# Performance work log

Hardware: AMD Instinct MI355X
Metric: run time of the kernel (lower is better)

## Reference

```python
import jax, jax.numpy as jnp
import numpy as np

NUM_CLASSES = 80
INF = 1e8
STRIDES = (8, 16, 32, 64, 128)
REG = ((0.0, 64.0), (64.0, 128.0), (128.0, 256.0), (256.0, 512.0), (512.0, INF))
GRAY_F = (0.9, 1.1)
FM = ((128, 128), (64, 64), (32, 32), (16, 16), (8, 8))  # 1024x1024 input


def _build_level_constants():
    pts, rr, gr, st = [], [], [], []
    for (h, w), s, (lo, up) in zip(FM, STRIDES, REG):
        xs = np.arange(w, dtype=np.float32) * s
        ys = np.arange(h, dtype=np.float32) * s
        ym, xm = np.meshgrid(ys, xs, indexing='ij')
        n = h * w
        pts.append(np.stack([xm.ravel(), ym.ravel()], axis=-1))
        rr.append(np.tile(np.array([lo, up], np.float32), (n, 1)))
        gr.append(np.tile(np.array([lo * GRAY_F[0], up * GRAY_F[1]], np.float32), (n, 1)))
        st.append(np.full((n,), s, np.float32))
    cat = lambda a: jnp.asarray(np.concatenate(a, axis=0))
    return cat(pts), cat(rr), cat(gr), cat(st)


def setup_inputs() -> dict:
    key = jax.random.key(0)
    k1, k2, k3, k4 = jax.random.split(key, 4)
    B, G = 8, 100
    x0 = jax.random.uniform(k1, (B, G, 1), minval=0.0, maxval=900.0)
    y0 = jax.random.uniform(k2, (B, G, 1), minval=0.0, maxval=900.0)
    wh = jax.random.uniform(k3, (B, G, 2), minval=8.0, maxval=512.0)
    gt_bboxes = jnp.concatenate([x0, y0, wh], axis=-1)  # xywh
    gt_labels = jax.random.randint(k4, (B, G), 0, NUM_CLASSES)
    points, reg_ranges, gray_ranges, strides = _build_level_constants()
    return dict(gt_bboxes=gt_bboxes, gt_labels=gt_labels, points=points,
                reg_ranges=reg_ranges, gray_ranges=gray_ranges, strides=strides)


def _single_image(gt_bboxes, gt_labels, points, reg_ranges, gray_ranges, strides):
    # gt_bboxes [G,4] (x,y,w,h); points [P,2]; returns [P, C+4]
    px = points[:, 0:1]                      # [P,1]
    py = points[:, 1:2]
    x0 = gt_bboxes[None, :, 0]               # [1,G]
    y0 = gt_bboxes[None, :, 1]
    w = gt_bboxes[None, :, 2]
    h = gt_bboxes[None, :, 3]
    cx = x0 + w / 2.0
    cy = y0 + h / 2.0
    half = strides[:, None] / 2.0            # [P,1]

    xs = jnp.abs(px - cx) / half
    xs = jnp.where(xs >= 1.0, xs, 1.0)       # == xs*(xs>=1) + (xs<1)
    ys = jnp.abs(py - cy) / half
    ys = jnp.where(ys >= 1.0, ys, 1.0)
    scores = jnp.sqrt(1.0 / xs) * jnp.sqrt(1.0 / ys)   # [P,G]

    dx1 = px - x0
    dy1 = py - y0
    dx2 = x0 + w - 1.0 - px
    dy2 = y0 + h - 1.0 - py
    delta = jnp.stack([dx1, dy1, dx2, dy2], axis=-1)   # [P,G,4]
    delta = delta / reg_ranges[:, 1][:, None, None]

    larger = jnp.maximum(w, h)               # [1,G]
    lo, up = reg_ranges[:, 0:1], reg_ranges[:, 1:2]      # [P,1]
    glo, gup = gray_ranges[:, 0:1], gray_ranges[:, 1:2]
    hit = jnp.min(delta, axis=-1) >= 0       # [P,G]
    green = (lo <= larger) & (larger <= up) & hit
    gray = (((glo <= larger) & (larger < lo)) | ((up < larger) & (larger <= gup))) & hit

    order = jnp.argsort(scores, axis=1)      # ascending, like torch.sort
    s_scores = jnp.take_along_axis(scores, order, axis=1)
    s_labels = jnp.take_along_axis(jnp.broadcast_to(gt_labels[None, :], scores.shape), order, axis=1)
    s_green = jnp.take_along_axis(green, order, axis=1)
    s_gray = jnp.take_along_axis(gray, order, axis=1)
    s_delta = jnp.take_along_axis(delta, order[..., None], axis=1)

    P = points.shape[0]
    rows = jnp.broadcast_to(jnp.arange(P)[:, None], s_labels.shape)
    cls = jnp.zeros((P, NUM_CLASSES), scores.dtype)
    cls = cls.at[rows, s_labels].max(jnp.where(s_green, s_scores, 0.0))
    gray_hit = jnp.zeros((P, NUM_CLASSES), scores.dtype)
    gray_hit = gray_hit.at[rows, s_labels].max(s_gray.astype(scores.dtype))
    cls = jnp.where(gray_hit > 0, -1.0, cls)  # gray writes happen after green

    filt = s_scores * (s_green & ~s_gray)
    sel = jnp.argmax(filt, axis=1)            # first max, like torch.max
    reg = jnp.take_along_axis(s_delta, sel[:, None, None], axis=1)[:, 0, :]  # [P,4]
    return jnp.concatenate([cls, reg], axis=-1)


def reference(gt_bboxes, gt_labels, points, reg_ranges, gray_ranges, strides):
    f = jax.vmap(lambda b, l: _single_image(b, l, points, reg_ranges, gray_ranges, strides))
    return f(gt_bboxes, gt_labels)
```

## Files before the change

### kernel.cpp

```cpp
#include <hip/hip_runtime.h>

#define ROWF 84

__global__ __launch_bounds__(256) void lfd_zero_kernel(float4* __restrict__ dst, int n4) {
    const int stride = gridDim.x * blockDim.x;
    const float4 z = make_float4(0.f, 0.f, 0.f, 0.f);
    for (int i = blockIdx.x * blockDim.x + threadIdx.x; i < n4; i += stride)
        dst[i] = z;
}

__global__ __launch_bounds__(64) void lfd_patch_kernel(
    const float* __restrict__ gt_bboxes,
    const int*   __restrict__ gt_labels,
    const float* __restrict__ points,
    const float* __restrict__ reg_ranges,
    const float* __restrict__ gray_ranges,
    const float* __restrict__ strides,
    float* __restrict__ out,
    int G, int P)
{
    extern __shared__ float lds[];
    float4*   boxA  = (float4*)lds;
    float2*   ctr   = (float2*)(boxA + G);
    unsigned* clist = (unsigned*)(ctr + ((G + 1) & ~1));

    const int tid = threadIdx.x;
    const int b   = blockIdx.y;
    const int p   = blockIdx.x * 64 + tid;

    const float px  = points[p * 2 + 0];
    const float py  = points[p * 2 + 1];
    const float lo  = reg_ranges[p * 2 + 0];
    const float up  = reg_ranges[p * 2 + 1];
    const float glo = gray_ranges[p * 2 + 0];
    const float gup = gray_ranges[p * 2 + 1];
    const float inv_half = 2.0f / strides[p];
    const float inv_up   = 1.0f / up;

    bool i0 = false, gray0 = false, i1 = false, gray1 = false;
    int  lab0 = 0, lab1 = 0;
    {
        int g = tid;
        if (g < G) {
            const float4 bb = *(const float4*)(gt_bboxes + (size_t)(b * G + g) * 4);
            boxA[g] = make_float4(bb.x, bb.y, bb.x + bb.z - 1.0f, bb.y + bb.w - 1.0f);
            ctr[g]  = make_float2(bb.x + 0.5f * bb.z, bb.y + 0.5f * bb.w);
            const float larger = fmaxf(bb.z, bb.w);
            lab0 = gt_labels[b * G + g];
            const bool green = (lo <= larger) && (larger <= up);
            gray0 = ((glo <= larger) && (larger < lo)) || ((up < larger) && (larger <= gup));
            i0 = green || gray0;
        }
        g = tid + 64;
        if (g < G) {
            const float4 bb = *(const float4*)(gt_bboxes + (size_t)(b * G + g) * 4);
            boxA[g] = make_float4(bb.x, bb.y, bb.x + bb.z - 1.0f, bb.y + bb.w - 1.0f);
            ctr[g]  = make_float2(bb.x + 0.5f * bb.z, bb.y + 0.5f * bb.w);
            const float larger = fmaxf(bb.z, bb.w);
            lab1 = gt_labels[b * G + g];
            const bool green = (lo <= larger) && (larger <= up);
            gray1 = ((glo <= larger) && (larger < lo)) || ((up < larger) && (larger <= gup));
            i1 = green || gray1;
        }
    }
    const unsigned long long m0 = __ballot(i0);
    const unsigned long long m1 = __ballot(i1);
    const int c0 = __popcll(m0);
    const unsigned long long below = (1ull << tid) - 1ull;
    if (i0) clist[__popcll(m0 & below)] =
        (unsigned)tid | ((unsigned)lab0 << 8) | (gray0 ? 0x80000000u : 0u);
    if (i1) clist[c0 + __popcll(m1 & below)] =
        (unsigned)(tid + 64) | ((unsigned)lab1 << 8) | (gray1 ? 0x80000000u : 0u);
    const int ncomp = c0 + __popcll(m1);

#define SC(X, Y) rsqrtf(fmaxf(fabsf(px - (X)) * inv_half, 1.0f) * \
                        fmaxf(fabsf(py - (Y)) * inv_half, 1.0f))
    const float4* ctr2 = (const float4*)ctr;
    float ms0 = 1e30f, ms1 = 1e30f, ms2 = 1e30f, ms3 = 1e30f;
    int   mg0 = 0, mg1 = 0, mg2 = 0, mg3 = 0;
    int g = 0;
    for (; g + 8 <= G; g += 8) {
        const float4 ca = ctr2[(g >> 1) + 0];
        const float4 cb = ctr2[(g >> 1) + 1];
        const float4 cc = ctr2[(g >> 1) + 2];
        const float4 cd = ctr2[(g >> 1) + 3];
        float s;
        s = SC(ca.x, ca.y); if (s < ms0) { ms0 = s; mg0 = g + 0; }
        s = SC(ca.z, ca.w); if (s < ms0) { ms0 = s; mg0 = g + 1; }
        s = SC(cb.x, cb.y); if (s < ms1) { ms1 = s; mg1 = g + 2; }
        s = SC(cb.z, cb.w); if (s < ms1) { ms1 = s; mg1 = g + 3; }
        s = SC(cc.x, cc.y); if (s < ms2) { ms2 = s; mg2 = g + 4; }
        s = SC(cc.z, cc.w); if (s < ms2) { ms2 = s; mg2 = g + 5; }
        s = SC(cd.x, cd.y); if (s < ms3) { ms3 = s; mg3 = g + 6; }
        s = SC(cd.z, cd.w); if (s < ms3) { ms3 = s; mg3 = g + 7; }
    }
    for (; g + 2 <= G; g += 2) {
        const float4 ca = ctr2[g >> 1];
        float s;
        s = SC(ca.x, ca.y); if (s < ms0) { ms0 = s; mg0 = g; }
        s = SC(ca.z, ca.w); if (s < ms0) { ms0 = s; mg0 = g + 1; }
    }
    if (g < G) {
        const float2 c = ctr[g];
        const float s = SC(c.x, c.y);
        if (s < ms0) { ms0 = s; mg0 = g; }
    }
    float min_score = ms0; int min_g = mg0;
    if (ms1 < min_score || (ms1 == min_score && mg1 < min_g)) { min_score = ms1; min_g = mg1; }
    if (ms2 < min_score || (ms2 == min_score && mg2 < min_g)) { min_score = ms2; min_g = mg2; }
    if (ms3 < min_score || (ms3 == min_score && mg3 < min_g)) { min_score = ms3; min_g = mg3; }

    float* myout = out + ((size_t)b * P + p) * ROWF;
    float best_score = 0.f; int best_g = 0;
    unsigned gm0 = 0u, gm1 = 0u, gm2 = 0u;
    for (int i = 0; i < ncomp; ++i) {
        const unsigned e = clist[i];
        const int gg = (int)(e & 0xFFu);
        const float4 A = boxA[gg];
        const float d1 = px - A.x, d2 = py - A.y, d3 = A.z - px, d4 = A.w - py;
        if (fminf(fminf(d1, d2), fminf(d3, d4)) >= 0.0f) {
            const int label = (int)((e >> 8) & 0x7Fu);
            if (e & 0x80000000u) {
                if (label < 32)      gm0 |= 1u << label;
                else if (label < 64) gm1 |= 1u << (label - 32);
                else                 gm2 |= 1u << (label - 64);
            } else {
                const float2 c = ctr[gg];
                const float s = SC(c.x, c.y);
                atomicMax((int*)(myout + label), __float_as_int(s));
                if (s > best_score) { best_score = s; best_g = gg; }
            }
        }
    }
#undef SC

    asm volatile("s_waitcnt vmcnt(0)" ::: "memory");

    unsigned t;
    t = gm0; while (t) { const int c = __ffs(t) - 1; myout[c]      = -1.0f; t &= t - 1u; }
    t = gm1; while (t) { const int c = __ffs(t) - 1; myout[32 + c] = -1.0f; t &= t - 1u; }
    t = gm2; while (t) { const int c = __ffs(t) - 1; myout[64 + c] = -1.0f; t &= t - 1u; }

    const int sel = (best_score > 0.f) ? best_g : min_g;
    const float4 A = boxA[sel];
    *(float4*)(myout + 80) = make_float4((px - A.x) * inv_up, (py - A.y) * inv_up,
                                         (A.z - px) * inv_up, (A.w - py) * inv_up);
}

extern "C" void kernel_launch(void* const* d_in, const int* in_sizes, int n_in,
                              void* d_out, int out_size, void* d_ws, size_t ws_size,
                              hipStream_t stream) {
    const float* gt_bboxes   = (const float*)d_in[0];
    const int*   gt_labels   = (const int*)d_in[1];
    const float* points      = (const float*)d_in[2];
    const float* reg_ranges  = (const float*)d_in[3];
    const float* gray_ranges = (const float*)d_in[4];
    const float* strides     = (const float*)d_in[5];
    float* out = (float*)d_out;

    const int P = in_sizes[5];
    const int B = out_size / (P * ROWF);
    const int G = in_sizes[1] / B;

    const int n4 = out_size / 4;
    lfd_zero_kernel<<<1024, 256, 0, stream>>>((float4*)out, n4);

    dim3 grid(P / 64, B);
    dim3 block(64);
    const size_t shmem = (size_t)G * sizeof(float4)
                       + (size_t)((G + 1) & ~1) * sizeof(float2)
                       + (size_t)G * sizeof(unsigned);
    lfd_patch_kernel<<<grid, block, shmem, stream>>>(
        gt_bboxes, gt_labels, points, reg_ranges, gray_ranges, strides, out, G, P);
}
```

Baseline: 41.98 us.

## Fuse zero-fill into main kernel with LDS-staged coalesced row writes

Removes the separate zero-fill kernel and the per-label global atomicMax/scatter writes. Each thread records hit and gray bitmasks plus regression targets in LDS. The block then writes its full output tile with coalesced float4 stores, recomputing per-class max scores from the bitmasks. This avoids writing the output twice and avoids scattered atomics, in exchange for redundant score recomputation and extra LDS use.

```diff
diff --git a/kernel.cpp b/kernel.cpp
--- a/kernel.cpp
+++ b/kernel.cpp
@@ -1,15 +1,9 @@
 #include <hip/hip_runtime.h>
 
 #define ROWF 84
-
-__global__ __launch_bounds__(256) void lfd_zero_kernel(float4* __restrict__ dst, int n4) {
-    const int stride = gridDim.x * blockDim.x;
-    const float4 z = make_float4(0.f, 0.f, 0.f, 0.f);
-    for (int i = blockIdx.x * blockDim.x + threadIdx.x; i < n4; i += stride)
-        dst[i] = z;
-}
-
-__global__ __launch_bounds__(64) void lfd_patch_kernel(
+#define RSTRIDE 17
+
+__global__ __launch_bounds__(64) void lfd_kernel(
     const float* __restrict__ gt_bboxes,
     const int*   __restrict__ gt_labels,
     const float* __restrict__ points,
@@ -23,6 +17,7 @@
     float4*   boxA  = (float4*)lds;
     float2*   ctr   = (float2*)(boxA + G);
     unsigned* clist = (unsigned*)(ctr + ((G + 1) & ~1));
+    unsigned* rowd  = clist + G;
 
     const int tid = threadIdx.x;
     const int b   = blockIdx.y;
@@ -110,9 +105,9 @@
     if (ms2 < min_score || (ms2 == min_score && mg2 < min_g)) { min_score = ms2; min_g = mg2; }
     if (ms3 < min_score || (ms3 == min_score && mg3 < min_g)) { min_score = ms3; min_g = mg3; }
 
-    float* myout = out + ((size_t)b * P + p) * ROWF;
+    unsigned hm0 = 0u, hm1 = 0u, hm2 = 0u, hm3 = 0u;
+    unsigned gm0 = 0u, gm1 = 0u, gm2 = 0u;
     float best_score = 0.f; int best_g = 0;
-    unsigned gm0 = 0u, gm1 = 0u, gm2 = 0u;
     for (int i = 0; i < ncomp; ++i) {
         const unsigned e = clist[i];
         const int gg = (int)(e & 0xFFu);
@@ -125,26 +120,77 @@
                 else if (label < 64) gm1 |= 1u << (label - 32);
                 else                 gm2 |= 1u << (label - 64);
             } else {
+                if (i < 32)       hm0 |= 1u << i;
+                else if (i < 64)  hm1 |= 1u << (i - 32);
+                else if (i < 96)  hm2 |= 1u << (i - 64);
+                else              hm3 |= 1u << (i - 96);
                 const float2 c = ctr[gg];
                 const float s = SC(c.x, c.y);
-                atomicMax((int*)(myout + label), __float_as_int(s));
                 if (s > best_score) { best_score = s; best_g = gg; }
             }
         }
     }
-#undef SC
-
-    asm volatile("s_waitcnt vmcnt(0)" ::: "memory");
-
-    unsigned t;
-    t = gm0; while (t) { const int c = __ffs(t) - 1; myout[c]      = -1.0f; t &= t - 1u; }
-    t = gm1; while (t) { const int c = __ffs(t) - 1; myout[32 + c] = -1.0f; t &= t - 1u; }
-    t = gm2; while (t) { const int c = __ffs(t) - 1; myout[64 + c] = -1.0f; t &= t - 1u; }
 
     const int sel = (best_score > 0.f) ? best_g : min_g;
     const float4 A = boxA[sel];
-    *(float4*)(myout + 80) = make_float4((px - A.x) * inv_up, (py - A.y) * inv_up,
-                                         (A.z - px) * inv_up, (A.w - py) * inv_up);
+    unsigned* my = rowd + tid * RSTRIDE;
+    my[0] = hm0; my[1] = hm1; my[2] = hm2; my[3] = hm3;
+    my[4] = gm0; my[5] = gm1; my[6] = gm2;
+    my[7] = __float_as_uint(px);
+    my[8] = __float_as_uint(py);
+    my[9] = __float_as_uint(inv_half);
+    my[10] = __float_as_uint((px - A.x) * inv_up);
+    my[11] = __float_as_uint((py - A.y) * inv_up);
+    my[12] = __float_as_uint((A.z - px) * inv_up);
+    my[13] = __float_as_uint((A.w - py) * inv_up);
+
+    float4* out4 = (float4*)(out + ((size_t)b * P + (size_t)blockIdx.x * 64) * ROWF);
+#pragma unroll
+    for (int k = 0; k < 21; ++k) {
+        const int j = k * 64 + tid;
+        const unsigned r = (unsigned)j / 21u;
+        const int s = j - 21 * (int)r;
+        const unsigned* rb = rowd + r * RSTRIDE;
+        float4 v;
+        if (s == 20) {
+            v = make_float4(__uint_as_float(rb[10]), __uint_as_float(rb[11]),
+                            __uint_as_float(rb[12]), __uint_as_float(rb[13]));
+        } else {
+            const int cbase = 4 * s;
+            const float px_r = __uint_as_float(rb[7]);
+            const float py_r = __uint_as_float(rb[8]);
+            const float ih_r = __uint_as_float(rb[9]);
+            float v0 = 0.f, v1 = 0.f, v2 = 0.f, v3 = 0.f;
+#pragma unroll
+            for (int w = 0; w < 4; ++w) {
+                unsigned m = rb[w];
+                while (m) {
+                    const int bit = __ffs(m) - 1; m &= m - 1u;
+                    const unsigned e = clist[w * 32 + bit];
+                    const unsigned lab = (e >> 8) & 0x7Fu;
+                    if ((int)(lab >> 2) == s) {
+                        const float2 c = ctr[e & 0xFFu];
+                        const float sc = rsqrtf(fmaxf(fabsf(px_r - c.x) * ih_r, 1.0f) *
+                                                fmaxf(fabsf(py_r - c.y) * ih_r, 1.0f));
+                        const unsigned l2 = lab & 3u;
+                        v0 = (l2 == 0u) ? fmaxf(v0, sc) : v0;
+                        v1 = (l2 == 1u) ? fmaxf(v1, sc) : v1;
+                        v2 = (l2 == 2u) ? fmaxf(v2, sc) : v2;
+                        v3 = (l2 == 3u) ? fmaxf(v3, sc) : v3;
+                    }
+                }
+            }
+            const unsigned gw = rb[4 + (s >> 3)];
+            const int sh = cbase & 31;
+            v0 = ((gw >> (sh + 0)) & 1u) ? -1.0f : v0;
+            v1 = ((gw >> (sh + 1)) & 1u) ? -1.0f : v1;
+            v2 = ((gw >> (sh + 2)) & 1u) ? -1.0f : v2;
+            v3 = ((gw >> (sh + 3)) & 1u) ? -1.0f : v3;
+            v = make_float4(v0, v1, v2, v3);
+        }
+        out4[j] = v;
+    }
+#undef SC
 }
 
 extern "C" void kernel_launch(void* const* d_in, const int* in_sizes, int n_in,
@@ -162,14 +208,12 @@
     const int B = out_size / (P * ROWF);
     const int G = in_sizes[1] / B;
 
-    const int n4 = out_size / 4;
-    lfd_zero_kernel<<<1024, 256, 0, stream>>>((float4*)out, n4);
-
     dim3 grid(P / 64, B);
     dim3 block(64);
     const size_t shmem = (size_t)G * sizeof(float4)
                        + (size_t)((G + 1) & ~1) * sizeof(float2)
-                       + (size_t)G * sizeof(unsigned);
-    lfd_patch_kernel<<<grid, block, shmem, stream>>>(
+                       + (size_t)G * sizeof(unsigned)
+                       + (size_t)(64 * RSTRIDE) * sizeof(unsigned);
+    lfd_kernel<<<grid, block, shmem, stream>>>(
         gt_bboxes, gt_labels, points, reg_ranges, gray_ranges, strides, out, G, P);
 }
```

New measurement: 85.82 us. +104.5%, slower.

## Fuse zeroing into single kernel with register class accumulators and full-row stores

Applied to the files above, without the earlier changes.

Drops the separate zero-fill kernel. Each thread keeps the 80 class scores in a register array, updated through a wave-uniform switch on the label, and writes the whole 84-float row with vectorized stores instead of global atomics plus scattered -1 writes. Blocks grow to 256 threads, and the candidate list is built once per block behind barriers. The cost is heavy register pressure from the 80-entry array and the switch, which may spill or cut occupancy. The readfirstlane assumes the list entry is uniform across the wave, which holds because every thread in the block reads the same shared list.

```diff
diff --git a/kernel.cpp b/kernel.cpp
--- a/kernel.cpp
+++ b/kernel.cpp
@@ -1,15 +1,9 @@
 #include <hip/hip_runtime.h>
 
 #define ROWF 84
+#define SENT 0xFFFFFFFFu
 
-__global__ __launch_bounds__(256) void lfd_zero_kernel(float4* __restrict__ dst, int n4) {
-    const int stride = gridDim.x * blockDim.x;
-    const float4 z = make_float4(0.f, 0.f, 0.f, 0.f);
-    for (int i = blockIdx.x * blockDim.x + threadIdx.x; i < n4; i += stride)
-        dst[i] = z;
-}
-
-__global__ __launch_bounds__(64) void lfd_patch_kernel(
+__global__ __launch_bounds__(256) void lfd_kernel(
     const float* __restrict__ gt_bboxes,
     const int*   __restrict__ gt_labels,
     const float* __restrict__ points,
@@ -19,63 +13,63 @@
     float* __restrict__ out,
     int G, int P)
 {
-    extern __shared__ float lds[];
-    float4*   boxA  = (float4*)lds;
-    float2*   ctr   = (float2*)(boxA + G);
-    unsigned* clist = (unsigned*)(ctr + ((G + 1) & ~1));
+    __shared__ float4   boxA[128];
+    __shared__ float4   ctrq[64];
+    __shared__ unsigned clist[128];
+    __shared__ unsigned flags[128];
+    __shared__ int      s_ncomp;
 
     const int tid = threadIdx.x;
     const int b   = blockIdx.y;
-    const int p   = blockIdx.x * 64 + tid;
+    const int p   = blockIdx.x * 256 + tid;
+    const bool active = (p < P);
+    const int  pc = active ? p : (P - 1);
 
-    const float px  = points[p * 2 + 0];
-    const float py  = points[p * 2 + 1];
-    const float lo  = reg_ranges[p * 2 + 0];
-    const float up  = reg_ranges[p * 2 + 1];
-    const float glo = gray_ranges[p * 2 + 0];
-    const float gup = gray_ranges[p * 2 + 1];
-    const float inv_half = 2.0f / strides[p];
+    const float px  = points[pc * 2 + 0];
+    const float py  = points[pc * 2 + 1];
+    const float lo  = reg_ranges[pc * 2 + 0];
+    const float up  = reg_ranges[pc * 2 + 1];
+    const float glo = gray_ranges[pc * 2 + 0];
+    const float gup = gray_ranges[pc * 2 + 1];
+    const float inv_half = 2.0f / strides[pc];
     const float inv_up   = 1.0f / up;
 
-    bool i0 = false, gray0 = false, i1 = false, gray1 = false;
-    int  lab0 = 0, lab1 = 0;
-    {
-        int g = tid;
-        if (g < G) {
-            const float4 bb = *(const float4*)(gt_bboxes + (size_t)(b * G + g) * 4);
-            boxA[g] = make_float4(bb.x, bb.y, bb.x + bb.z - 1.0f, bb.y + bb.w - 1.0f);
-            ctr[g]  = make_float2(bb.x + 0.5f * bb.z, bb.y + 0.5f * bb.w);
+    if (tid < 128) {
+        unsigned f = SENT;
+        if (tid < G) {
+            const float4 bb = *(const float4*)(gt_bboxes + ((size_t)b * G + tid) * 4);
+            boxA[tid] = make_float4(bb.x, bb.y, bb.x + bb.z - 1.0f, bb.y + bb.w - 1.0f);
+            ((float2*)ctrq)[tid] = make_float2(bb.x + 0.5f * bb.z, bb.y + 0.5f * bb.w);
             const float larger = fmaxf(bb.z, bb.w);
-            lab0 = gt_labels[b * G + g];
+            const int lab = gt_labels[b * G + tid];
             const bool green = (lo <= larger) && (larger <= up);
-            gray0 = ((glo <= larger) && (larger < lo)) || ((up < larger) && (larger <= gup));
-            i0 = green || gray0;
+            const bool gray  = ((glo <= larger) && (larger < lo)) ||
+                               ((up < larger) && (larger <= gup));
+            if (green || gray)
+                f = (unsigned)tid | ((unsigned)lab << 8) | (gray ? 0x80000000u : 0u);
         }
-        g = tid + 64;
-        if (g < G) {
-            const float4 bb = *(const float4*)(gt_bboxes + (size_t)(b * G + g) * 4);
-            boxA[g] = make_float4(bb.x, bb.y, bb.x + bb.z - 1.0f, bb.y + bb.w - 1.0f);
-            ctr[g]  = make_float2(bb.x + 0.5f * bb.z, bb.y + 0.5f * bb.w);
-            const float larger = fmaxf(bb.z, bb.w);
-            lab1 = gt_labels[b * G + g];
-            const bool green = (lo <= larger) && (larger <= up);
-            gray1 = ((glo <= larger) && (larger < lo)) || ((up < larger) && (larger <= gup));
-            i1 = green || gray1;
-        }
+        flags[tid] = f;
     }
-    const unsigned long long m0 = __ballot(i0);
-    const unsigned long long m1 = __ballot(i1);
-    const int c0 = __popcll(m0);
-    const unsigned long long below = (1ull << tid) - 1ull;
-    if (i0) clist[__popcll(m0 & below)] =
-        (unsigned)tid | ((unsigned)lab0 << 8) | (gray0 ? 0x80000000u : 0u);
-    if (i1) clist[c0 + __popcll(m1 & below)] =
-        (unsigned)(tid + 64) | ((unsigned)lab1 << 8) | (gray1 ? 0x80000000u : 0u);
-    const int ncomp = c0 + __popcll(m1);
+    __syncthreads();
+
+    if (tid < 64) {
+        const unsigned f0 = flags[tid], f1 = flags[tid + 64];
+        const bool i0 = (f0 != SENT), i1 = (f1 != SENT);
+        const unsigned long long m0 = __ballot(i0);
+        const unsigned long long m1 = __ballot(i1);
+        const unsigned long long below = (1ull << tid) - 1ull;
+        const int c0 = __popcll(m0);
+        if (i0) clist[__popcll(m0 & below)] = f0;
+        if (i1) clist[c0 + __popcll(m1 & below)] = f1;
+        if (tid == 0) s_ncomp = c0 + __popcll(m1);
+    }
+    __syncthreads();
+    const int ncomp = s_ncomp;
 
 #define SC(X, Y) rsqrtf(fmaxf(fabsf(px - (X)) * inv_half, 1.0f) * \
                         fmaxf(fabsf(py - (Y)) * inv_half, 1.0f))
-    const float4* ctr2 = (const float4*)ctr;
+    const float4* ctr2 = (const float4*)ctrq;
+    const float2* ctr  = (const float2*)ctrq;
     float ms0 = 1e30f, ms1 = 1e30f, ms2 = 1e30f, ms3 = 1e30f;
     int   mg0 = 0, mg1 = 0, mg2 = 0, mg3 = 0;
     int g = 0;
@@ -110,41 +104,66 @@
     if (ms2 < min_score || (ms2 == min_score && mg2 < min_g)) { min_score = ms2; min_g = mg2; }
     if (ms3 < min_score || (ms3 == min_score && mg3 < min_g)) { min_score = ms3; min_g = mg3; }
 
-    float* myout = out + ((size_t)b * P + p) * ROWF;
+    float acc[80];
+#pragma unroll
+    for (int i = 0; i < 80; ++i) acc[i] = 0.f;
+    unsigned gm0 = 0u, gm1 = 0u, gm2 = 0u;
     float best_score = 0.f; int best_g = 0;
-    unsigned gm0 = 0u, gm1 = 0u, gm2 = 0u;
+
+    unsigned e = (ncomp > 0) ? clist[0] : 0u;
     for (int i = 0; i < ncomp; ++i) {
-        const unsigned e = clist[i];
-        const int gg = (int)(e & 0xFFu);
+        const unsigned enext = (i + 1 < ncomp) ? clist[i + 1] : 0u;
+        const unsigned eu  = (unsigned)__builtin_amdgcn_readfirstlane((int)e);
+        const int gg  = (int)(eu & 0xFFu);
+        const int lab = (int)((eu >> 8) & 0x7Fu);
         const float4 A = boxA[gg];
+        const float2 c = ctr[gg];
         const float d1 = px - A.x, d2 = py - A.y, d3 = A.z - px, d4 = A.w - py;
-        if (fminf(fminf(d1, d2), fminf(d3, d4)) >= 0.0f) {
-            const int label = (int)((e >> 8) & 0x7Fu);
-            if (e & 0x80000000u) {
-                if (label < 32)      gm0 |= 1u << label;
-                else if (label < 64) gm1 |= 1u << (label - 32);
-                else                 gm2 |= 1u << (label - 64);
-            } else {
-                const float2 c = ctr[gg];
-                const float s = SC(c.x, c.y);
-                atomicMax((int*)(myout + label), __float_as_int(s));
-                if (s > best_score) { best_score = s; best_g = gg; }
+        const bool hit = fminf(fminf(d1, d2), fminf(d3, d4)) >= 0.0f;
+        if (eu & 0x80000000u) {
+            const unsigned bit = 1u << (lab & 31);
+            if (lab < 32)      gm0 |= hit ? bit : 0u;
+            else if (lab < 64) gm1 |= hit ? bit : 0u;
+            else               gm2 |= hit ? bit : 0u;
+        } else {
+            float s = SC(c.x, c.y);
+            s = hit ? s : 0.0f;
+            switch (lab) {
+#define CS(L) case L: acc[L] = fmaxf(acc[L], s); break;
+            CS(0) CS(1) CS(2) CS(3) CS(4) CS(5) CS(6) CS(7) CS(8) CS(9)
+            CS(10) CS(11) CS(12) CS(13) CS(14) CS(15) CS(16) CS(17) CS(18) CS(19)
+            CS(20) CS(21) CS(22) CS(23) CS(24) CS(25) CS(26) CS(27) CS(28) CS(29)
+            CS(30) CS(31) CS(32) CS(33) CS(34) CS(35) CS(36) CS(37) CS(38) CS(39)
+            CS(40) CS(41) CS(42) CS(43) CS(44) CS(45) CS(46) CS(47) CS(48) CS(49)
+            CS(50) CS(51) CS(52) CS(53) CS(54) CS(55) CS(56) CS(57) CS(58) CS(59)
+            CS(60) CS(61) CS(62) CS(63) CS(64) CS(65) CS(66) CS(67) CS(68) CS(69)
+            CS(70) CS(71) CS(72) CS(73) CS(74) CS(75) CS(76) CS(77) CS(78) CS(79)
+#undef CS
             }
+            if (s > best_score) { best_score = s; best_g = gg; }
         }
+        e = enext;
+    }
+
+    if (active) {
+        const int sel = (best_score > 0.f) ? best_g : min_g;
+        const float4 A = boxA[sel];
+        float4* out4 = (float4*)(out + ((size_t)b * P + p) * ROWF);
+#pragma unroll
+        for (int k = 0; k < 20; ++k) {
+            const unsigned gw = (k < 8) ? gm0 : ((k < 16) ? gm1 : gm2);
+            const int sh = (4 * k) & 31;
+            float4 v;
+            v.x = ((gw >> (sh + 0)) & 1u) ? -1.0f : acc[4 * k + 0];
+            v.y = ((gw >> (sh + 1)) & 1u) ? -1.0f : acc[4 * k + 1];
+            v.z = ((gw >> (sh + 2)) & 1u) ? -1.0f : acc[4 * k + 2];
+            v.w = ((gw >> (sh + 3)) & 1u) ? -1.0f : acc[4 * k + 3];
+            out4[k] = v;
+        }
+        out4[20] = make_float4((px - A.x) * inv_up, (py - A.y) * inv_up,
+                               (A.z - px) * inv_up, (A.w - py) * inv_up);
     }
 #undef SC
-
-    asm volatile("s_waitcnt vmcnt(0)" ::: "memory");
-
-    unsigned t;
-    t = gm0; while (t) { const int c = __ffs(t) - 1; myout[c]      = -1.0f; t &= t - 1u; }
-    t = gm1; while (t) { const int c = __ffs(t) - 1; myout[32 + c] = -1.0f; t &= t - 1u; }
-    t = gm2; while (t) { const int c = __ffs(t) - 1; myout[64 + c] = -1.0f; t &= t - 1u; }
-
-    const int sel = (best_score > 0.f) ? best_g : min_g;
-    const float4 A = boxA[sel];
-    *(float4*)(myout + 80) = make_float4((px - A.x) * inv_up, (py - A.y) * inv_up,
-                                         (A.z - px) * inv_up, (A.w - py) * inv_up);
 }
 
 extern "C" void kernel_launch(void* const* d_in, const int* in_sizes, int n_in,
@@ -162,14 +181,8 @@
     const int B = out_size / (P * ROWF);
     const int G = in_sizes[1] / B;
 
-    const int n4 = out_size / 4;
-    lfd_zero_kernel<<<1024, 256, 0, stream>>>((float4*)out, n4);
-
-    dim3 grid(P / 64, B);
-    dim3 block(64);
-    const size_t shmem = (size_t)G * sizeof(float4)
-                       + (size_t)((G + 1) & ~1) * sizeof(float2)
-                       + (size_t)G * sizeof(unsigned);
-    lfd_patch_kernel<<<grid, block, shmem, stream>>>(
+    dim3 grid((P + 255) / 256, B);
+    dim3 block(256);
+    lfd_kernel<<<grid, block, 0, stream>>>(
         gt_bboxes, gt_labels, points, reg_ranges, gray_ranges, strides, out, G, P);
 }
```

Measured after the change: 76.25 us. 1.82x slower.

## Fuse output zeroing into main kernel and accumulate class maxima in registers

Applied to the files above, without the earlier changes.

Removes the separate zero-fill kernel: each block now zeroes its own 64-row output tile before computing. Green and gray candidates are split into separate LDS lists. Per-label maxima are kept in a small register slot table (8 entries) instead of global atomicMax, falling back to atomics only on overflow, and gray labels are masked out before the write. This saves one kernel launch and most of the global atomics, at the cost of extra register pressure and fixed-size LDS arrays that assume G at most 128.

```diff
diff --git a/kernel.cpp b/kernel.cpp
--- a/kernel.cpp
+++ b/kernel.cpp
@@ -1,15 +1,9 @@
 #include <hip/hip_runtime.h>
 
 #define ROWF 84
-
-__global__ __launch_bounds__(256) void lfd_zero_kernel(float4* __restrict__ dst, int n4) {
-    const int stride = gridDim.x * blockDim.x;
-    const float4 z = make_float4(0.f, 0.f, 0.f, 0.f);
-    for (int i = blockIdx.x * blockDim.x + threadIdx.x; i < n4; i += stride)
-        dst[i] = z;
-}
-
-__global__ __launch_bounds__(64) void lfd_patch_kernel(
+#define KSLOT 8
+
+__global__ __launch_bounds__(64) void lfd_kernel(
     const float* __restrict__ gt_bboxes,
     const int*   __restrict__ gt_labels,
     const float* __restrict__ points,
@@ -19,14 +13,20 @@
     float* __restrict__ out,
     int G, int P)
 {
-    extern __shared__ float lds[];
-    float4*   boxA  = (float4*)lds;
-    float2*   ctr   = (float2*)(boxA + G);
-    unsigned* clist = (unsigned*)(ctr + ((G + 1) & ~1));
+    __shared__ float4   boxA[128];
+    __shared__ float4   ctrq[64];
+    __shared__ unsigned glist[128];
+    __shared__ unsigned rlist[128];
 
     const int tid = threadIdx.x;
     const int b   = blockIdx.y;
     const int p   = blockIdx.x * 64 + tid;
+
+    float4* blk4 = (float4*)(out + ((size_t)b * P + (size_t)blockIdx.x * 64) * ROWF);
+    const float4 z = make_float4(0.f, 0.f, 0.f, 0.f);
+#pragma unroll
+    for (int k = 0; k < 21; ++k)
+        blk4[k * 64 + tid] = z;
 
     const float px  = points[p * 2 + 0];
     const float py  = points[p * 2 + 1];
@@ -37,45 +37,48 @@
     const float inv_half = 2.0f / strides[p];
     const float inv_up   = 1.0f / up;
 
-    bool i0 = false, gray0 = false, i1 = false, gray1 = false;
+    bool gr0 = false, gy0 = false, gr1 = false, gy1 = false;
     int  lab0 = 0, lab1 = 0;
     {
         int g = tid;
         if (g < G) {
             const float4 bb = *(const float4*)(gt_bboxes + (size_t)(b * G + g) * 4);
             boxA[g] = make_float4(bb.x, bb.y, bb.x + bb.z - 1.0f, bb.y + bb.w - 1.0f);
-            ctr[g]  = make_float2(bb.x + 0.5f * bb.z, bb.y + 0.5f * bb.w);
+            ((float2*)ctrq)[g] = make_float2(bb.x + 0.5f * bb.z, bb.y + 0.5f * bb.w);
             const float larger = fmaxf(bb.z, bb.w);
             lab0 = gt_labels[b * G + g];
-            const bool green = (lo <= larger) && (larger <= up);
-            gray0 = ((glo <= larger) && (larger < lo)) || ((up < larger) && (larger <= gup));
-            i0 = green || gray0;
+            gr0 = (lo <= larger) && (larger <= up);
+            gy0 = ((glo <= larger) && (larger < lo)) || ((up < larger) && (larger <= gup));
         }
         g = tid + 64;
         if (g < G) {
             const float4 bb = *(const float4*)(gt_bboxes + (size_t)(b * G + g) * 4);
             boxA[g] = make_float4(bb.x, bb.y, bb.x + bb.z - 1.0f, bb.y + bb.w - 1.0f);
-            ctr[g]  = make_float2(bb.x + 0.5f * bb.z, bb.y + 0.5f * bb.w);
+            ((float2*)ctrq)[g] = make_float2(bb.x + 0.5f * bb.z, bb.y + 0.5f * bb.w);
             const float larger = fmaxf(bb.z, bb.w);
             lab1 = gt_labels[b * G + g];
-            const bool green = (lo <= larger) && (larger <= up);
-            gray1 = ((glo <= larger) && (larger < lo)) || ((up < larger) && (larger <= gup));
-            i1 = green || gray1;
-        }
-    }
-    const unsigned long long m0 = __ballot(i0);
-    const unsigned long long m1 = __ballot(i1);
-    const int c0 = __popcll(m0);
+            gr1 = (lo <= larger) && (larger <= up);
+            gy1 = ((glo <= larger) && (larger < lo)) || ((up < larger) && (larger <= gup));
+        }
+    }
+    const unsigned long long bg0 = __ballot(gr0);
+    const unsigned long long bg1 = __ballot(gr1);
+    const unsigned long long br0 = __ballot(gy0);
+    const unsigned long long br1 = __ballot(gy1);
     const unsigned long long below = (1ull << tid) - 1ull;
-    if (i0) clist[__popcll(m0 & below)] =
-        (unsigned)tid | ((unsigned)lab0 << 8) | (gray0 ? 0x80000000u : 0u);
-    if (i1) clist[c0 + __popcll(m1 & below)] =
-        (unsigned)(tid + 64) | ((unsigned)lab1 << 8) | (gray1 ? 0x80000000u : 0u);
-    const int ncomp = c0 + __popcll(m1);
+    if (gr0) glist[__popcll(bg0 & below)] = (unsigned)tid | ((unsigned)lab0 << 8);
+    if (gr1) glist[__popcll(bg0) + __popcll(bg1 & below)] =
+        (unsigned)(tid + 64) | ((unsigned)lab1 << 8);
+    const int ng = __popcll(bg0) + __popcll(bg1);
+    if (gy0) rlist[__popcll(br0 & below)] = (unsigned)tid | ((unsigned)lab0 << 8);
+    if (gy1) rlist[__popcll(br0) + __popcll(br1 & below)] =
+        (unsigned)(tid + 64) | ((unsigned)lab1 << 8);
+    const int nr = __popcll(br0) + __popcll(br1);
 
 #define SC(X, Y) rsqrtf(fmaxf(fabsf(px - (X)) * inv_half, 1.0f) * \
                         fmaxf(fabsf(py - (Y)) * inv_half, 1.0f))
-    const float4* ctr2 = (const float4*)ctr;
+    const float4* ctr2 = (const float4*)ctrq;
+    const float2* ctr  = (const float2*)ctrq;
     float ms0 = 1e30f, ms1 = 1e30f, ms2 = 1e30f, ms3 = 1e30f;
     int   mg0 = 0, mg1 = 0, mg2 = 0, mg3 = 0;
     int g = 0;
@@ -110,32 +113,69 @@
     if (ms2 < min_score || (ms2 == min_score && mg2 < min_g)) { min_score = ms2; min_g = mg2; }
     if (ms3 < min_score || (ms3 == min_score && mg3 < min_g)) { min_score = ms3; min_g = mg3; }
 
-    float* myout = out + ((size_t)b * P + p) * ROWF;
-    float best_score = 0.f; int best_g = 0;
     unsigned gm0 = 0u, gm1 = 0u, gm2 = 0u;
-    for (int i = 0; i < ncomp; ++i) {
-        const unsigned e = clist[i];
+    for (int i = 0; i < nr; ++i) {
+        const unsigned e = rlist[i];
         const int gg = (int)(e & 0xFFu);
         const float4 A = boxA[gg];
         const float d1 = px - A.x, d2 = py - A.y, d3 = A.z - px, d4 = A.w - py;
         if (fminf(fminf(d1, d2), fminf(d3, d4)) >= 0.0f) {
-            const int label = (int)((e >> 8) & 0x7Fu);
-            if (e & 0x80000000u) {
-                if (label < 32)      gm0 |= 1u << label;
-                else if (label < 64) gm1 |= 1u << (label - 32);
-                else                 gm2 |= 1u << (label - 64);
-            } else {
-                const float2 c = ctr[gg];
-                const float s = SC(c.x, c.y);
-                atomicMax((int*)(myout + label), __float_as_int(s));
-                if (s > best_score) { best_score = s; best_g = gg; }
+            const int lab = (int)(e >> 8);
+            if (lab < 32)      gm0 |= 1u << lab;
+            else if (lab < 64) gm1 |= 1u << (lab - 32);
+            else               gm2 |= 1u << (lab - 64);
+        }
+    }
+
+    asm volatile("s_waitcnt vmcnt(0)" ::: "memory");
+
+    float* myout = out + ((size_t)b * P + p) * ROWF;
+    int   slab[KSLOT];
+    float sval[KSLOT];
+#pragma unroll
+    for (int j = 0; j < KSLOT; ++j) { slab[j] = -1; sval[j] = 0.f; }
+    int cnt = 0; bool spill = false;
+    float best_score = 0.f; int best_g = 0;
+
+    for (int i = 0; i < ng; ++i) {
+        const unsigned e = glist[i];
+        const int gg = (int)(e & 0xFFu);
+        const float4 A = boxA[gg];
+        const float d1 = px - A.x, d2 = py - A.y, d3 = A.z - px, d4 = A.w - py;
+        if (fminf(fminf(d1, d2), fminf(d3, d4)) >= 0.0f) {
+            const int lab = (int)(e >> 8);
+            const float2 c = ctr[gg];
+            const float s = SC(c.x, c.y);
+            bool placed = false;
+#pragma unroll
+            for (int j = 0; j < KSLOT; ++j)
+                if (slab[j] == lab) { sval[j] = fmaxf(sval[j], s); placed = true; }
+            if (!placed) {
+                if (cnt < KSLOT) {
+#pragma unroll
+                    for (int j = 0; j < KSLOT; ++j)
+                        if (cnt == j) { slab[j] = lab; sval[j] = s; }
+                    ++cnt;
+                } else {
+                    spill = true;
+                    atomicMax((int*)(myout + lab), __float_as_int(s));
+                }
             }
-        }
-    }
-#undef SC
-
-    asm volatile("s_waitcnt vmcnt(0)" ::: "memory");
-
+            if (s > best_score) { best_score = s; best_g = gg; }
+        }
+    }
+    if (__any(spill))
+        asm volatile("s_waitcnt vmcnt(0)" ::: "memory");
+
+#pragma unroll
+    for (int j = 0; j < KSLOT; ++j) {
+        if (j < cnt) {
+            const int L = slab[j];
+            const unsigned gmask = (L < 32) ? gm0 : ((L < 64) ? gm1 : gm2);
+            if (!((gmask >> (L & 31)) & 1u))
+                myout[L] = sval[j];
+        }
+    }
     unsigned t;
     t = gm0; while (t) { const int c = __ffs(t) - 1; myout[c]      = -1.0f; t &= t - 1u; }
     t = gm1; while (t) { const int c = __ffs(t) - 1; myout[32 + c] = -1.0f; t &= t - 1u; }
@@ -145,6 +185,7 @@
     const float4 A = boxA[sel];
     *(float4*)(myout + 80) = make_float4((px - A.x) * inv_up, (py - A.y) * inv_up,
                                          (A.z - px) * inv_up, (A.w - py) * inv_up);
+#undef SC
 }
 
 extern "C" void kernel_launch(void* const* d_in, const int* in_sizes, int n_in,
@@ -162,14 +203,8 @@
     const int B = out_size / (P * ROWF);
     const int G = in_sizes[1] / B;
 
-    const int n4 = out_size / 4;
-    lfd_zero_kernel<<<1024, 256, 0, stream>>>((float4*)out, n4);
-
     dim3 grid(P / 64, B);
     dim3 block(64);
-    const size_t shmem = (size_t)G * sizeof(float4)
-                       + (size_t)((G + 1) & ~1) * sizeof(float2)
-                       + (size_t)G * sizeof(unsigned);
-    lfd_patch_kernel<<<grid, block, shmem, stream>>>(
+    lfd_kernel<<<grid, block, 0, stream>>>(
         gt_bboxes, gt_labels, points, reg_ranges, gray_ranges, strides, out, G, P);
 }
```

Measured after the change: 48.84 us. 1.16x slower.
